# Kernel tuning notes

Measured on AMD Instinct MI355X. Metric: run time of the kernel, lower is better.

Reference implementation:

```python
import jax, jax.numpy as jnp
import numpy as np
from jax import lax

K = 3
STRIDE = 1
PAD = 1


def _active_sites(mask):
    # mask: [B, Cm, H, W] int. A patch is 'active' if ANY element of the
    # unfolded (im2col) patch is nonzero -> max-pool of (mask != 0) over the
    # same kernel/stride/padding window.
    m = jnp.any(mask != 0, axis=1, keepdims=True).astype(jnp.float32)  # [B,1,H,W]
    pooled = lax.reduce_window(
        m, 0.0, lax.max,
        window_dimensions=(1, 1, K, K),
        window_strides=(1, 1, STRIDE, STRIDE),
        padding=((0, 0), (0, 0), (PAD, PAD), (PAD, PAD)))
    return pooled > 0  # [B,1,H_out,W_out] bool


def reference(x, mask, weight, bias):
    # Faithful math of MyConv: conv2d(x, weight) + bias at active patch sites
    # (patches whose mask window contains any nonzero), exact zeros elsewhere.
    # masked_scatter in the original preserves patch order, so this equals
    # active * (conv + bias).
    conv = lax.conv_general_dilated(
        x, weight,
        window_strides=(STRIDE, STRIDE),
        padding=((PAD, PAD), (PAD, PAD)),
        dimension_numbers=('NCHW', 'OIHW', 'NCHW'))  # [B,C_out,H_out,W_out]
    active = _active_sites(mask)
    out = (conv + bias[None, :, None, None]) * active.astype(conv.dtype)
    return out


def setup_inputs() -> dict:
    key = jax.random.key(0)
    k1, k2, k3, k4 = jax.random.split(key, 4)
    B, C_in, C_out, H, W = 8, 128, 128, 128, 128
    x = jax.random.normal(k1, (B, C_in, H, W), dtype=jnp.float32)
    mask = jax.random.randint(k2, (B, 1, H, W), 0, 2, dtype=jnp.int32)
    fan_in = C_in * K * K
    bound = 1.0 / np.sqrt(fan_in)
    weight = jax.random.uniform(k3, (C_out, C_in, K, K), minval=-bound, maxval=bound, dtype=jnp.float32)
    bias = jax.random.uniform(k4, (C_out,), minval=-bound, maxval=bound, dtype=jnp.float32)
    return {"x": x, "mask": mask, "weight": weight, "bias": bias}
```

## Files before the change

### kernel.cpp

```cpp
#include <hip/hip_runtime.h>


typedef __bf16 bf16x8 __attribute__((ext_vector_type(8)));
typedef unsigned short u16x8 __attribute__((ext_vector_type(8)));
typedef float f32x4 __attribute__((ext_vector_type(4)));

__device__ __forceinline__ unsigned short f2bf(float f) {
    unsigned int u = __float_as_uint(f);
    u += 0x7fffu + ((u >> 16) & 1u);
    return (unsigned short)(u >> 16);
}

__global__ void setup_wp(const float* __restrict__ wgt, unsigned short* __restrict__ wpp) {
    const int e    = blockIdx.x * 256 + threadIdx.x;
    const int j    = e & 31;
    const int m    = (e >> 5) & 127;
    const int r    = e >> 12;
    const int kw   = r - (r / 3) * 3;
    const int cbkh = r / 3;
    const int cb   = cbkh & 3;
    const int kh   = cbkh >> 2;
    const int ci   = 4 * (j & 7) + (j >> 3);
    wpp[e] = f2bf(wgt[((m * 128 + cb * 32 + ci) * 3 + kh) * 3 + kw]);
}

__device__ __forceinline__ void stage_conv(const float* __restrict__ x,
                                           unsigned char* XsN,
                                           int b, int cb, int hb, int t) {
    const u16x8 z  = {0, 0, 0, 0, 0, 0, 0, 0};
    const int rr   = t + 1;
    const int cswz = (rr + (rr >> 2)) & 3;
    #pragma unroll
    for (int y = 0; y < 2; ++y) {
        const int h    = hb + y;
        const bool inb = (unsigned)h < 128u;
        const float* xr = x + ((((b * 128 + cb * 32) * 128) + h) << 7) + t;
        #pragma unroll
        for (int lc = 0; lc < 4; ++lc) {
            u16x8 o = z;
            if (inb) {
                #pragma unroll
                for (int s = 0; s < 8; ++s)
                    o[s] = f2bf(xr[(lc << 14) + (s << 16)]);
            }
            *(u16x8*)(XsN + y * 8320 + rr * 64 + ((lc ^ cswz) << 4)) = o;
        }
    }
}

__global__ __launch_bounds__(128, 2)
void myconv11(const float* __restrict__ x,
              const int* __restrict__ mask,
              const unsigned short* __restrict__ wp,
              const float* __restrict__ bias,
              float* __restrict__ out)
{
    __shared__ __align__(16) unsigned char Xs[2][16640];
    __shared__ float act[256];

    const int t = threadIdx.x;
    const int b     = blockIdx.x & 7;
    const int r8    = blockIdx.x >> 3;
    const int mhalf = r8 & 1;
    const int h0    = (r8 >> 1) << 1;

    const int lane = t & 63;
    const int l16  = lane & 15;
    const int q    = lane >> 4;
    const int g    = t >> 6;

    if (t < 32) {
        const u16x8 z = {0, 0, 0, 0, 0, 0, 0, 0};
        const int bf = (t >> 4) & 1;
        const int y  = (t >> 3) & 1;
        const int rr = ((t >> 2) & 1) ? 129 : 0;
        const int c  = t & 3;
        *(u16x8*)(&Xs[bf][0] + y * 8320 + rr * 64 + (c << 4)) = z;
    }

    stage_conv(x, &Xs[0][0], b, 0, h0 - 1, t);

    #pragma unroll
    for (int gg = 0; gg < 2; ++gg) {
        const int h = h0 + gg;
        int any = 0;
        #pragma unroll
        for (int kh = 0; kh < 3; ++kh) {
            int hh = h + kh - 1;
            if ((unsigned)hh < 128u) {
                const int* mrow = mask + (b * 128 + hh) * 128;
                #pragma unroll
                for (int kw = 0; kw < 3; ++kw) {
                    int ww = t + kw - 1;
                    if ((unsigned)ww < 128u) any |= mrow[ww];
                }
            }
        }
        act[gg * 128 + t] = any ? 1.0f : 0.0f;
    }

    int bb[3];
    #pragma unroll
    for (int kw = 0; kw < 3; ++kw) {
        const int rr   = l16 + kw;
        const int slot = q ^ ((rr + (rr >> 2)) & 3);
        bb[kw] = g * 8320 + rr * 64 + (slot << 4);
    }

    const unsigned char* agl = (const unsigned char*)wp + (mhalf * 64 + l16) * 64 + q * 16;

    f32x4 acc[4][8];
    const f32x4 fzero = {0.f, 0.f, 0.f, 0.f};
    #pragma unroll
    for (int i = 0; i < 4; ++i)
        #pragma unroll
        for (int j = 0; j < 8; ++j)
            acc[i][j] = fzero;

    __syncthreads();

    for (int r = 0; r < 12; ++r) {
        if (r < 11) {
            const int rn = r + 1;
            stage_conv(x, &Xs[rn & 1][0], b, rn & 3, h0 + (rn >> 2) - 1, t);
        }

        const unsigned char* ar = agl + r * 24576;
        const unsigned char* xb = &Xs[r & 1][0];
        #pragma unroll
        for (int kw = 0; kw < 3; ++kw) {
            bf16x8 af[4];
            #pragma unroll
            for (int i = 0; i < 4; ++i)
                af[i] = *(const bf16x8*)(ar + kw * 8192 + i * 1024);
            bf16x8 bfr[8];
            #pragma unroll
            for (int j = 0; j < 8; ++j)
                bfr[j] = *(const bf16x8*)(xb + bb[kw] + j * 1024);
            #pragma unroll
            for (int i = 0; i < 4; ++i)
                #pragma unroll
                for (int j = 0; j < 8; ++j)
                    acc[i][j] = __builtin_amdgcn_mfma_f32_16x16x32_bf16(af[i], bfr[j], acc[i][j], 0, 0, 0);
        }

        __syncthreads();
    }

    #pragma unroll
    for (int i = 0; i < 4; ++i) {
        const int m0 = mhalf * 64 + (i << 4) + (q << 2);
        const f32x4 bv = *(const f32x4*)(bias + m0);
        #pragma unroll
        for (int j = 0; j < 8; ++j) {
            const int w = (j << 4) + l16;
            const float a = act[(g << 7) + w];
            float* base = out + (((b << 7) + m0) << 14) + ((h0 + g) << 7) + w;
            #pragma unroll
            for (int rg = 0; rg < 4; ++rg)
                base[rg << 14] = (acc[i][j][rg] + bv[rg]) * a;
        }
    }
}

#define LDAF 40
__global__ __launch_bounds__(256, 2)
void myconv_fb(const float* __restrict__ x,
               const int* __restrict__ mask,
               const float* __restrict__ wgt,
               const float* __restrict__ bias,
               float* __restrict__ out)
{
    __shared__ unsigned short As[128 * LDAF];
    __shared__ unsigned short Bs[128 * LDAF];
    __shared__ float act[128];

    const int t   = threadIdx.x;
    const int blk = blockIdx.x;
    const int b   = blk >> 7;
    const int h   = blk & 127;

    if (t < 128) {
        int any = 0;
        #pragma unroll
        for (int kh = 0; kh < 3; ++kh) {
            int hh = h + kh - 1;
            if ((unsigned)hh < 128u) {
                const int* mrow = mask + (b * 128 + hh) * 128;
                #pragma unroll
                for (int kw = 0; kw < 3; ++kw) {
                    int ww = t + kw - 1;
                    if ((unsigned)ww < 128u) any |= mrow[ww];
                }
            }
        }
        act[t] = any ? 1.0f : 0.0f;
    }

    const int lane = t & 63;
    const int l16  = lane & 15;
    const int half = lane >> 4;
    const int wv   = t >> 6;
    const int wm   = (wv >> 1) << 6;
    const int wn   = (wv & 1) << 6;

    f32x4 acc[4][4];
    const f32x4 fzero = {0.f, 0.f, 0.f, 0.f};
    #pragma unroll
    for (int i = 0; i < 4; ++i)
        #pragma unroll
        for (int j = 0; j < 4; ++j)
            acc[i][j] = fzero;

    const int am  = t >> 3;
    const int ac4 = (t & 7) << 2;
    const int n     = t & 127;
    const int khalf = __builtin_amdgcn_readfirstlane(t >> 7);
    const int xb    = b << 21;

    for (int kt = 0; kt < 36; ++kt) {
        __syncthreads();
        #pragma unroll
        for (int jj = 0; jj < 4; ++jj) {
            const int m = am + (jj << 5);
            const float4 v = *(const float4*)(wgt + m * 1152 + kt * 32 + ac4);
            unsigned short* dst = &As[m * LDAF + ac4];
            dst[0] = f2bf(v.x); dst[1] = f2bf(v.y); dst[2] = f2bf(v.z); dst[3] = f2bf(v.w);
        }
        u16x8 bv0, bv1;
        #pragma unroll
        for (int s = 0; s < 16; ++s) {
            const int k  = kt * 32 + khalf * 16 + s;
            const int ci = (k * 7282) >> 16;
            const int r  = k - ci * 9;
            const int kh = (r >= 3) + (r >= 6);
            const int kw = r - kh * 3;
            const int hh = h + kh - 1;
            float v = 0.f;
            if ((unsigned)hh < 128u) {
                const int ww = n + kw - 1;
                if ((unsigned)ww < 128u)
                    v = x[xb + (ci << 14) + (hh << 7) + ww];
            }
            if (s < 8) bv0[s] = f2bf(v); else bv1[s - 8] = f2bf(v);
        }
        *(u16x8*)&Bs[n * LDAF + khalf * 16]     = bv0;
        *(u16x8*)&Bs[n * LDAF + khalf * 16 + 8] = bv1;

        __syncthreads();

        bf16x8 af[4], bfr[4];
        #pragma unroll
        for (int i = 0; i < 4; ++i)
            af[i] = *(const bf16x8*)&As[(wm + (i << 4) + l16) * LDAF + (half << 3)];
        #pragma unroll
        for (int j = 0; j < 4; ++j)
            bfr[j] = *(const bf16x8*)&Bs[(wn + (j << 4) + l16) * LDAF + (half << 3)];
        #pragma unroll
        for (int i = 0; i < 4; ++i)
            #pragma unroll
            for (int j = 0; j < 4; ++j)
                acc[i][j] = __builtin_amdgcn_mfma_f32_16x16x32_bf16(af[i], bfr[j], acc[i][j], 0, 0, 0);
    }

    #pragma unroll
    for (int i = 0; i < 4; ++i) {
        #pragma unroll
        for (int j = 0; j < 4; ++j) {
            const int ncol = wn + (j << 4) + l16;
            const float a  = act[ncol];
            #pragma unroll
            for (int rg = 0; rg < 4; ++rg) {
                const int m = wm + (i << 4) + (half << 2) + rg;
                out[(((b << 7) + m) << 14) + (h << 7) + ncol] =
                    (acc[i][j][rg] + bias[m]) * a;
            }
        }
    }
}

extern "C" void kernel_launch(void* const* d_in, const int* in_sizes, int n_in,
                              void* d_out, int out_size, void* d_ws, size_t ws_size,
                              hipStream_t stream) {
    const float* x    = (const float*)d_in[0];
    const int*   mask = (const int*)d_in[1];
    const float* wgt  = (const float*)d_in[2];
    const float* bias = (const float*)d_in[3];
    float* out        = (float*)d_out;

    const size_t WP_ELEMS = 36ull * 128 * 32;
    if (ws_size >= WP_ELEMS * 2) {
        unsigned short* wpw = (unsigned short*)d_ws;
        setup_wp<<<dim3(576), dim3(256), 0, stream>>>(wgt, wpw);
        myconv11<<<dim3(1024), dim3(128), 0, stream>>>(x, mask, wpw, bias, out);
    } else {
        myconv_fb<<<dim3(1024), dim3(256), 0, stream>>>(x, mask, wgt, bias, out);
    }
}
```

Baseline: 162.6 us.

## Merge output-channel halves into one 256-thread block sharing staged input rows

Each block now computes both 64-channel halves with 256 threads instead of splitting them across two 128-thread blocks, so each staged input slab is converted and loaded once rather than twice. The input is staged as four per-row slabs reused across the three kh taps, with a rolling refill schedule synchronized per kh step. This cuts redundant global reads and fp32-to-bf16 conversions but halves the grid, adds more barriers per channel block, and leaves less double-buffering slack between staging and MFMA work.

```diff
diff --git a/kernel.cpp b/kernel.cpp
--- a/kernel.cpp
+++ b/kernel.cpp
@@ -24,65 +24,59 @@
     wpp[e] = f2bf(wgt[((m * 128 + cb * 32 + ci) * 3 + kh) * 3 + kw]);
 }
 
-__device__ __forceinline__ void stage_conv(const float* __restrict__ x,
-                                           unsigned char* XsN,
-                                           int b, int cb, int hb, int t) {
-    const u16x8 z  = {0, 0, 0, 0, 0, 0, 0, 0};
-    const int rr   = t + 1;
+__device__ __forceinline__ void stage1(const float* __restrict__ x,
+                                       unsigned char* slab,
+                                       int b, int cb, int h, int t) {
+    const int rr   = (t & 127) + 1;
     const int cswz = (rr + (rr >> 2)) & 3;
-    #pragma unroll
-    for (int y = 0; y < 2; ++y) {
-        const int h    = hb + y;
-        const bool inb = (unsigned)h < 128u;
-        const float* xr = x + ((((b * 128 + cb * 32) * 128) + h) << 7) + t;
-        #pragma unroll
-        for (int lc = 0; lc < 4; ++lc) {
-            u16x8 o = z;
-            if (inb) {
-                #pragma unroll
-                for (int s = 0; s < 8; ++s)
-                    o[s] = f2bf(xr[(lc << 14) + (s << 16)]);
-            }
-            *(u16x8*)(XsN + y * 8320 + rr * 64 + ((lc ^ cswz) << 4)) = o;
-        }
-    }
-}
-
-__global__ __launch_bounds__(128, 2)
-void myconv11(const float* __restrict__ x,
+    const int lc0  = (t >> 7) << 1;
+    const bool inb = (unsigned)h < 128u;
+    const float* xr = x + ((((b * 128 + cb * 32) * 128) + h) << 7) + (rr - 1);
+    #pragma unroll
+    for (int d = 0; d < 2; ++d) {
+        const int lc = lc0 + d;
+        u16x8 o = {0, 0, 0, 0, 0, 0, 0, 0};
+        if (inb) {
+            #pragma unroll
+            for (int s = 0; s < 8; ++s)
+                o[s] = f2bf(xr[(lc << 14) + (s << 16)]);
+        }
+        *(u16x8*)(slab + rr * 64 + ((lc ^ cswz) << 4)) = o;
+    }
+}
+
+__global__ __launch_bounds__(256, 2)
+void myconv12(const float* __restrict__ x,
               const int* __restrict__ mask,
               const unsigned short* __restrict__ wp,
               const float* __restrict__ bias,
               float* __restrict__ out)
 {
-    __shared__ __align__(16) unsigned char Xs[2][16640];
+    __shared__ __align__(16) unsigned char Xs[4 * 8320];
     __shared__ float act[256];
 
     const int t = threadIdx.x;
-    const int b     = blockIdx.x & 7;
-    const int r8    = blockIdx.x >> 3;
-    const int mhalf = r8 & 1;
-    const int h0    = (r8 >> 1) << 1;
-
-    const int lane = t & 63;
-    const int l16  = lane & 15;
-    const int q    = lane >> 4;
-    const int g    = t >> 6;
+    const int b  = blockIdx.x & 7;
+    const int h0 = (blockIdx.x >> 3) << 1;
+
+    const int lane  = t & 63;
+    const int l16   = lane & 15;
+    const int q     = lane >> 4;
+    const int g     = (t >> 6) & 1;
+    const int mhalf = t >> 7;
 
     if (t < 32) {
         const u16x8 z = {0, 0, 0, 0, 0, 0, 0, 0};
-        const int bf = (t >> 4) & 1;
-        const int y  = (t >> 3) & 1;
-        const int rr = ((t >> 2) & 1) ? 129 : 0;
+        const int p  = t >> 3;
+        const int rr = (t & 4) ? 129 : 0;
         const int c  = t & 3;
-        *(u16x8*)(&Xs[bf][0] + y * 8320 + rr * 64 + (c << 4)) = z;
-    }
-
-    stage_conv(x, &Xs[0][0], b, 0, h0 - 1, t);
-
-    #pragma unroll
-    for (int gg = 0; gg < 2; ++gg) {
-        const int h = h0 + gg;
+        *(u16x8*)(&Xs[p * 8320] + rr * 64 + (c << 4)) = z;
+    }
+
+    {
+        const int gg = t >> 7;
+        const int w  = t & 127;
+        const int h  = h0 + gg;
         int any = 0;
         #pragma unroll
         for (int kh = 0; kh < 3; ++kh) {
@@ -91,20 +85,24 @@
                 const int* mrow = mask + (b * 128 + hh) * 128;
                 #pragma unroll
                 for (int kw = 0; kw < 3; ++kw) {
-                    int ww = t + kw - 1;
+                    int ww = w + kw - 1;
                     if ((unsigned)ww < 128u) any |= mrow[ww];
                 }
             }
         }
-        act[gg * 128 + t] = any ? 1.0f : 0.0f;
-    }
+        act[t] = any ? 1.0f : 0.0f;
+    }
+
+    #pragma unroll
+    for (int y = 0; y < 4; ++y)
+        stage1(x, &Xs[y * 8320], b, 0, h0 - 1 + y, t);
 
     int bb[3];
     #pragma unroll
     for (int kw = 0; kw < 3; ++kw) {
         const int rr   = l16 + kw;
         const int slot = q ^ ((rr + (rr >> 2)) & 3);
-        bb[kw] = g * 8320 + rr * 64 + (slot << 4);
+        bb[kw] = rr * 64 + (slot << 4);
     }
 
     const unsigned char* agl = (const unsigned char*)wp + (mhalf * 64 + l16) * 64 + q * 16;
@@ -119,33 +117,46 @@
 
     __syncthreads();
 
-    for (int r = 0; r < 12; ++r) {
-        if (r < 11) {
-            const int rn = r + 1;
-            stage_conv(x, &Xs[rn & 1][0], b, rn & 3, h0 + (rn >> 2) - 1, t);
-        }
-
-        const unsigned char* ar = agl + r * 24576;
-        const unsigned char* xb = &Xs[r & 1][0];
-        #pragma unroll
-        for (int kw = 0; kw < 3; ++kw) {
-            bf16x8 af[4];
-            #pragma unroll
-            for (int i = 0; i < 4; ++i)
-                af[i] = *(const bf16x8*)(ar + kw * 8192 + i * 1024);
-            bf16x8 bfr[8];
-            #pragma unroll
-            for (int j = 0; j < 8; ++j)
-                bfr[j] = *(const bf16x8*)(xb + bb[kw] + j * 1024);
-            #pragma unroll
-            for (int i = 0; i < 4; ++i)
-                #pragma unroll
-                for (int j = 0; j < 8; ++j)
-                    acc[i][j] = __builtin_amdgcn_mfma_f32_16x16x32_bf16(af[i], bfr[j], acc[i][j], 0, 0, 0);
-        }
-
-        __syncthreads();
-    }
+#define COMPUTE_KH(k)                                                          \
+    {                                                                          \
+        const unsigned char* ar = agl + ((k) * 4 + cb) * 24576;                \
+        const unsigned char* xb = &Xs[((k) + g) * 8320];                       \
+        _Pragma("unroll")                                                      \
+        for (int kw = 0; kw < 3; ++kw) {                                       \
+            bf16x8 af[4];                                                      \
+            _Pragma("unroll")                                                  \
+            for (int i = 0; i < 4; ++i)                                        \
+                af[i] = *(const bf16x8*)(ar + kw * 8192 + i * 1024);           \
+            bf16x8 bfr[8];                                                     \
+            _Pragma("unroll")                                                  \
+            for (int j = 0; j < 8; ++j)                                        \
+                bfr[j] = *(const bf16x8*)(xb + bb[kw] + j * 1024);             \
+            _Pragma("unroll")                                                  \
+            for (int i = 0; i < 4; ++i)                                        \
+                _Pragma("unroll")                                              \
+                for (int j = 0; j < 8; ++j)                                    \
+                    acc[i][j] = __builtin_amdgcn_mfma_f32_16x16x32_bf16(       \
+                        af[i], bfr[j], acc[i][j], 0, 0, 0);                    \
+        }                                                                      \
+    }
+
+    for (int cb = 0; cb < 4; ++cb) {
+        if (cb > 0) {
+            stage1(x, &Xs[2 * 8320], b, cb, h0 + 1, t);
+            stage1(x, &Xs[3 * 8320], b, cb, h0 + 2, t);
+        }
+        COMPUTE_KH(0);
+        __syncthreads();
+
+        if (cb < 3) stage1(x, &Xs[0 * 8320], b, cb + 1, h0 - 1, t);
+        COMPUTE_KH(1);
+        __syncthreads();
+
+        if (cb < 3) stage1(x, &Xs[1 * 8320], b, cb + 1, h0 + 0, t);
+        COMPUTE_KH(2);
+        __syncthreads();
+    }
+#undef COMPUTE_KH
 
     #pragma unroll
     for (int i = 0; i < 4; ++i) {
@@ -292,7 +303,7 @@
     if (ws_size >= WP_ELEMS * 2) {
         unsigned short* wpw = (unsigned short*)d_ws;
         setup_wp<<<dim3(576), dim3(256), 0, stream>>>(wgt, wpw);
-        myconv11<<<dim3(1024), dim3(128), 0, stream>>>(x, mask, wpw, bias, out);
+        myconv12<<<dim3(512), dim3(256), 0, stream>>>(x, mask, wpw, bias, out);
     } else {
         myconv_fb<<<dim3(1024), dim3(256), 0, stream>>>(x, mask, wgt, bias, out);
     }
```

Measured after the change: 139.9 us. -14.0%, faster.
